# Optimization experiments

Hardware: AMD Instinct MI355X
Metric: run time of the kernel (lower is better)

## Reference

```python
import jax, jax.numpy as jnp
import numpy as np

EMBED_DIM = 1024
NUM_HEADS = 16
HEAD_DIM = EMBED_DIM // NUM_HEADS


def setup_inputs() -> dict:
    key = jax.random.key(0)
    ks = jax.random.split(key, 6)
    B, S = 2, 2048
    x = jax.random.normal(ks[0], (B, S, EMBED_DIM), dtype=jnp.float32)
    # causal boolean mask, broadcast to (B, H, S, S)
    causal = jnp.tril(jnp.ones((S, S), dtype=bool))
    mask = jnp.broadcast_to(causal, (B, NUM_HEADS, S, S))
    s_in = 1.0 / np.sqrt(EMBED_DIM)
    qkv_w = jax.random.normal(ks[1], (3 * EMBED_DIM, EMBED_DIM), dtype=jnp.float32) * s_in
    qkv_b = jax.random.normal(ks[2], (3 * EMBED_DIM,), dtype=jnp.float32) * 0.01
    proj_w = jax.random.normal(ks[3], (EMBED_DIM, EMBED_DIM), dtype=jnp.float32) * s_in
    proj_b = jax.random.normal(ks[4], (EMBED_DIM,), dtype=jnp.float32) * 0.01
    return {"x": x, "mask": mask, "qkv_w": qkv_w, "qkv_b": qkv_b,
            "proj_w": proj_w, "proj_b": proj_b}


def reference(x, mask, qkv_w, qkv_b, proj_w, proj_b):
    B, S, E = x.shape
    H, D = NUM_HEADS, HEAD_DIM
    qkv = x @ qkv_w.T + qkv_b                     # (B, S, 3E)
    q, k, v = jnp.split(qkv, 3, axis=-1)
    # (B, H, S, D)
    q = q.reshape(B, S, H, D).transpose(0, 2, 1, 3)
    k = k.reshape(B, S, H, D).transpose(0, 2, 1, 3)
    v = v.reshape(B, S, H, D).transpose(0, 2, 1, 3)
    scale = D ** (-0.5)
    attn = jnp.einsum('bhqd,bhkd->bhqk', q, k) * scale
    attn = jnp.where(mask, attn, jnp.float32(-10000.0))
    attn = attn - jnp.max(attn, axis=-1, keepdims=True)
    attn = jax.nn.softmax(attn, axis=-1)
    attn = jnp.where(mask, attn, jnp.float32(0.0))
    # dropout is identity in eval mode
    out = jnp.einsum('bhqk,bhkd->bhqd', attn, v)
    out = out.transpose(0, 2, 1, 3).reshape(B, S, E)
    return out @ proj_w.T + proj_b
```

## Files before the change

kernel.cpp:

```cpp
#include <hip/hip_runtime.h>
#include <hip/hip_bf16.h>

#define BATCH 2
#define SEQ 2048
#define EMBED 1024
#define NHEADS 16
#define HDIM 64

typedef __hip_bfloat16 bf16;
typedef __attribute__((ext_vector_type(8))) short bf16x8;
typedef __attribute__((ext_vector_type(4))) short bf16x4;
typedef __attribute__((ext_vector_type(4))) float f32x4;

typedef const __attribute__((address_space(1))) void* gaddr_t;
typedef __attribute__((address_space(3))) void* laddr_t;

__device__ __forceinline__ bf16x8 lds_frag8(const bf16* p) {
    const bf16x4 a = *(const bf16x4*)p;
    const bf16x4 b = *(const bf16x4*)(p + 4);
    return __builtin_shufflevector(a, b, 0, 1, 2, 3, 4, 5, 6, 7);
}

__global__ __launch_bounds__(256)
void f2b_all(const float* __restrict__ s0, bf16* __restrict__ d0, int n0,
             const float* __restrict__ s1, bf16* __restrict__ d1, int n1,
             const float* __restrict__ s2, bf16* __restrict__ d2, int n2)
{
    int i = blockIdx.x * 256 + threadIdx.x;
    const float* s; bf16* d;
    if (i < n0)                { s = s0; d = d0; }
    else if ((i -= n0) < n1)   { s = s1; d = d1; }
    else if ((i -= n1) < n2)   { s = s2; d = d2; }
    else return;
    const float4 v = ((const float4*)s)[i];
    union { ushort4 u4; bf16 h[4]; } o;
    o.h[0] = __float2bfloat16(v.x);
    o.h[1] = __float2bfloat16(v.y);
    o.h[2] = __float2bfloat16(v.z);
    o.h[3] = __float2bfloat16(v.w);
    ((ushort4*)d)[i] = o.u4;
}

template<int MODE>
__global__ __launch_bounds__(256)
void gemm_bt(const bf16* __restrict__ A, const bf16* __restrict__ B,
             const float* __restrict__ bias, void* __restrict__ Cv,
             int M, int N, int K)
{
    __shared__ __align__(16) bf16 lA[128 * 32];
    __shared__ __align__(16) bf16 lB[128 * 32];
    const int tid  = threadIdx.x;
    const int bn   = blockIdx.x, bm = blockIdx.y;
    const int wave = tid >> 6, lane = tid & 63;
    const int wm   = (wave >> 1) << 6, wn = (wave & 1) << 6;
    const int quad = lane >> 4, l16 = lane & 15;

    f32x4 acc[4][4] = {};

    for (int kt = 0; kt < K; kt += 32) {
        __syncthreads();
        #pragma unroll
        for (int i = 0; i < 2; ++i) {
            const int c = tid + (i << 8);
            const int r = c >> 2, kc = (c & 3) << 3;
            const bf16* gA = A + (long)(bm * 128 + r) * K + (kt + kc);
            const bf16* gB = B + (long)(bn * 128 + r) * K + (kt + kc);
            __builtin_amdgcn_global_load_lds((gaddr_t)gA, (laddr_t)&lA[c << 3], 16, 0, 0);
            __builtin_amdgcn_global_load_lds((gaddr_t)gB, (laddr_t)&lB[c << 3], 16, 0, 0);
        }
        __syncthreads();

        bf16x8 af[4], bfr[4];
        #pragma unroll
        for (int t = 0; t < 4; ++t) {
            af[t]  = *(const bf16x8*)&lA[(wm + t * 16 + l16) * 32 + quad * 8];
            bfr[t] = *(const bf16x8*)&lB[(wn + t * 16 + l16) * 32 + quad * 8];
        }
        #pragma unroll
        for (int tm = 0; tm < 4; ++tm)
            #pragma unroll
            for (int tn = 0; tn < 4; ++tn)
                acc[tm][tn] = __builtin_amdgcn_mfma_f32_16x16x32_bf16(
                    af[tm], bfr[tn], acc[tm][tn], 0, 0, 0);
    }

    #pragma unroll
    for (int tm = 0; tm < 4; ++tm) {
        #pragma unroll
        for (int tn = 0; tn < 4; ++tn) {
            const int gn = bn * 128 + wn + tn * 16 + l16;
            const float bv = bias[gn];
            if (MODE == 0) {
                #pragma unroll
                for (int r = 0; r < 4; ++r) {
                    const int gm = bm * 128 + wm + tm * 16 + quad * 4 + r;
                    ((float*)Cv)[(long)gm * N + gn] = acc[tm][tn][r] + bv;
                }
            } else {
                const int part = gn >> 10, h = (gn >> 6) & (NHEADS - 1), d = gn & (HDIM - 1);
                const int gm0 = bm * 128 + wm + tm * 16 + quad * 4;
                const int b = gm0 >> 11, s0 = gm0 & (SEQ - 1);
                if (part == 2) {
                    union { ushort4 u4; bf16 hv[4]; } o;
                    #pragma unroll
                    for (int r = 0; r < 4; ++r) o.hv[r] = __float2bfloat16(acc[tm][tn][r] + bv);
                    const long off = ((((long)2 * BATCH + b) * NHEADS + h) * HDIM + d) * SEQ + s0;
                    *(ushort4*)((bf16*)Cv + off) = o.u4;
                } else {
                    #pragma unroll
                    for (int r = 0; r < 4; ++r) {
                        const long off = ((((long)part * BATCH + b) * NHEADS + h) * SEQ + (s0 + r)) * HDIM + d;
                        ((bf16*)Cv)[off] = __float2bfloat16(acc[tm][tn][r] + bv);
                    }
                }
            }
        }
    }
}

__global__ __launch_bounds__(256)
void attn_nf(const bf16* __restrict__ Q, const bf16* __restrict__ K,
             const bf16* __restrict__ Vt, bf16* __restrict__ O)
{
    __shared__ __align__(16) bf16 pS[4 * 32 * 68];

    const int tid  = threadIdx.x;
    const int wave = tid >> 6, lane = tid & 63;
    const int quad = lane >> 4, l15 = lane & 15;
    const int bh   = blockIdx.y;
    const int qg   = (15 - blockIdx.x) * 4 + wave;
    const int qw0  = qg * 32;

    const bf16* Qb  = Q  + (long)bh * SEQ * HDIM;
    const bf16* Kb  = K  + (long)bh * SEQ * HDIM;
    const bf16* Vtb = Vt + (long)bh * HDIM * SEQ;
    bf16* pW = pS + wave * 32 * 68;

    bf16x8 qf[2][2];
    #pragma unroll
    for (int mt = 0; mt < 2; ++mt)
        #pragma unroll
        for (int c = 0; c < 2; ++c) {
            union { int4 i; bf16x8 v; } u;
            u.i = *(const int4*)(Qb + (long)(qw0 + mt * 16 + l15) * HDIM + c * 32 + quad * 8);
            qf[mt][c] = u.v;
        }

    f32x4 acc[2][4] = {};
    float lsum[8] = {};

    const int nkt = (qw0 >> 6) + 1;
    const float sc = 0.125f * 1.44269504088896340736f;

    for (int t = 0; t < nkt; ++t) {
        const int kb = t * 64;

        f32x4 s[2][4] = {};
        #pragma unroll
        for (int c = 0; c < 2; ++c) {
            #pragma unroll
            for (int nt = 0; nt < 4; ++nt) {
                union { int4 i; bf16x8 v; } u;
                u.i = *(const int4*)(Kb + (long)(kb + nt * 16 + l15) * HDIM + c * 32 + quad * 8);
                #pragma unroll
                for (int mt = 0; mt < 2; ++mt)
                    s[mt][nt] = __builtin_amdgcn_mfma_f32_16x16x32_bf16(
                        qf[mt][c], u.v, s[mt][nt], 0, 0, 0);
            }
        }

        #pragma unroll
        for (int mt = 0; mt < 2; ++mt)
            #pragma unroll
            for (int nt = 0; nt < 4; ++nt)
                #pragma unroll
                for (int r = 0; r < 4; ++r) {
                    const int rl = mt * 16 + quad * 4 + r;
                    const int cl = nt * 16 + l15;
                    const float p = ((kb + cl) <= (qw0 + rl))
                        ? __builtin_amdgcn_exp2f(s[mt][nt][r] * sc) : 0.f;
                    lsum[mt * 4 + r] += p;
                    pW[rl * 68 + cl] = __float2bfloat16(p);
                }

        #pragma unroll
        for (int c = 0; c < 2; ++c) {
            bf16x8 pf[2];
            #pragma unroll
            for (int mt = 0; mt < 2; ++mt)
                pf[mt] = lds_frag8(&pW[(mt * 16 + l15) * 68 + c * 32 + quad * 8]);
            #pragma unroll
            for (int nt = 0; nt < 4; ++nt) {
                union { int4 i; bf16x8 v; } u;
                u.i = *(const int4*)(Vtb + (long)(nt * 16 + l15) * SEQ + kb + c * 32 + quad * 8);
                #pragma unroll
                for (int mt = 0; mt < 2; ++mt)
                    acc[mt][nt] = __builtin_amdgcn_mfma_f32_16x16x32_bf16(
                        pf[mt], u.v, acc[mt][nt], 0, 0, 0);
            }
        }
    }

    #pragma unroll
    for (int i = 0; i < 8; ++i) {
        #pragma unroll
        for (int m = 1; m < 16; m <<= 1) lsum[i] += __shfl_xor(lsum[i], m, 64);
        lsum[i] = 1.f / lsum[i];
    }

    const int b = bh >> 4, h = bh & 15;
    #pragma unroll
    for (int mt = 0; mt < 2; ++mt)
        #pragma unroll
        for (int r = 0; r < 4; ++r) {
            const int rl = mt * 16 + quad * 4 + r;
            bf16* orow = O + ((long)b * SEQ + (qw0 + rl)) * EMBED + h * HDIM;
            const float inv = lsum[mt * 4 + r];
            #pragma unroll
            for (int nt = 0; nt < 4; ++nt)
                orow[nt * 16 + l15] = __float2bfloat16(acc[mt][nt][r] * inv);
        }
}

extern "C" void kernel_launch(void* const* d_in, const int* in_sizes, int n_in,
                              void* d_out, int out_size, void* d_ws, size_t ws_size,
                              hipStream_t stream)
{
    const float* x      = (const float*)d_in[0];
    const float* qkv_w  = (const float*)d_in[2];
    const float* qkv_b  = (const float*)d_in[3];
    const float* proj_w = (const float*)d_in[4];
    const float* proj_b = (const float*)d_in[5];
    float* out = (float*)d_out;

    const long nX  = (long)BATCH * SEQ * EMBED;
    const long nQW = 3L * EMBED * EMBED;
    const long nPW = (long)EMBED * EMBED;
    const long per = (long)BATCH * NHEADS * SEQ * HDIM;

    bf16* xw  = (bf16*)d_ws;
    bf16* qwm = xw + nX;
    bf16* pwm = qwm + nQW;
    bf16* qw  = pwm + nPW;
    bf16* kw  = qw + per;
    bf16* vw  = kw + per;
    bf16* att = vw + per;

    const int n0 = (int)(nX / 4), n1 = (int)(nQW / 4), n2 = (int)(nPW / 4);
    f2b_all<<<(n0 + n1 + n2 + 255) / 256, 256, 0, stream>>>(
        x, xw, n0, qkv_w, qwm, n1, proj_w, pwm, n2);

    gemm_bt<1><<<dim3(3 * EMBED / 128, BATCH * SEQ / 128), 256, 0, stream>>>(
        xw, qwm, qkv_b, qw, BATCH * SEQ, 3 * EMBED, EMBED);

    attn_nf<<<dim3(16, BATCH * NHEADS), 256, 0, stream>>>(qw, kw, vw, att);

    gemm_bt<0><<<dim3(EMBED / 128, BATCH * SEQ / 128), 256, 0, stream>>>(
        att, pwm, proj_b, out, BATCH * SEQ, EMBED, EMBED);
}
```

Baseline: 765.9 us.

## Split attention key loop across two blocks and combine partial outputs

Each attention query tile is now processed by two blocks, each taking alternate key tiles, which doubles the grid to improve CU occupancy and load balance. Unnormalized fp32 partial outputs and row sums go to workspace, and a new combine kernel adds them, normalizes, and writes bf16 in the head-interleaved layout. This trades extra global traffic and an additional launch for more parallelism.

```diff
diff --git a/kernel.cpp b/kernel.cpp
--- a/kernel.cpp
+++ b/kernel.cpp
@@ -120,15 +120,18 @@
 
 __global__ __launch_bounds__(256)
 void attn_nf(const bf16* __restrict__ Q, const bf16* __restrict__ K,
-             const bf16* __restrict__ Vt, bf16* __restrict__ O)
+             const bf16* __restrict__ Vt, float* __restrict__ Op,
+             float* __restrict__ lp)
 {
     __shared__ __align__(16) bf16 pS[4 * 32 * 68];
 
     const int tid  = threadIdx.x;
     const int wave = tid >> 6, lane = tid & 63;
     const int quad = lane >> 4, l15 = lane & 15;
-    const int bh   = blockIdx.y;
-    const int qg   = (15 - blockIdx.x) * 4 + wave;
+    const int bh   = blockIdx.x;
+    const int half = blockIdx.y >> 4;
+    const int qidx = blockIdx.y & 15;
+    const int qg   = (15 - qidx) * 4 + wave;
     const int qw0  = qg * 32;
 
     const bf16* Qb  = Q  + (long)bh * SEQ * HDIM;
@@ -152,7 +155,7 @@
     const int nkt = (qw0 >> 6) + 1;
     const float sc = 0.125f * 1.44269504088896340736f;
 
-    for (int t = 0; t < nkt; ++t) {
+    for (int t = half; t < nkt; t += 2) {
         const int kb = t * 64;
 
         f32x4 s[2][4] = {};
@@ -202,24 +205,45 @@
     }
 
     #pragma unroll
-    for (int i = 0; i < 8; ++i) {
+    for (int i = 0; i < 8; ++i)
         #pragma unroll
         for (int m = 1; m < 16; m <<= 1) lsum[i] += __shfl_xor(lsum[i], m, 64);
-        lsum[i] = 1.f / lsum[i];
-    }
-
-    const int b = bh >> 4, h = bh & 15;
+
+    const long halfO = (long)BATCH * NHEADS * SEQ * HDIM;
+    float* Oh = Op + half * halfO + ((long)bh * SEQ) * HDIM;
+    float* lh = lp + half * (BATCH * NHEADS * SEQ) + bh * SEQ;
     #pragma unroll
     for (int mt = 0; mt < 2; ++mt)
         #pragma unroll
         for (int r = 0; r < 4; ++r) {
             const int rl = mt * 16 + quad * 4 + r;
-            bf16* orow = O + ((long)b * SEQ + (qw0 + rl)) * EMBED + h * HDIM;
-            const float inv = lsum[mt * 4 + r];
+            float* orow = Oh + (long)(qw0 + rl) * HDIM;
             #pragma unroll
             for (int nt = 0; nt < 4; ++nt)
-                orow[nt * 16 + l15] = __float2bfloat16(acc[mt][nt][r] * inv);
-        }
+                orow[nt * 16 + l15] = acc[mt][nt][r];
+            if (l15 == 0) lh[qw0 + rl] = lsum[mt * 4 + r];
+        }
+}
+
+__global__ __launch_bounds__(256)
+void attn_combine(const float* __restrict__ Op, const float* __restrict__ lp,
+                  bf16* __restrict__ att)
+{
+    const int i = blockIdx.x * 256 + threadIdx.x;
+    const int d4 = i & 15, q = (i >> 4) & (SEQ - 1), bh = i >> 15;
+    const long halfO = (long)BATCH * NHEADS * SEQ * HDIM;
+    const long rowo  = ((long)bh * SEQ + q) * HDIM;
+    const float4 a = ((const float4*)(Op + rowo))[d4];
+    const float4 b = ((const float4*)(Op + halfO + rowo))[d4];
+    const int li = bh * SEQ + q;
+    const float inv = 1.f / (lp[li] + lp[BATCH * NHEADS * SEQ + li]);
+    const int bb = bh >> 4, h = bh & 15;
+    union { ushort4 u4; bf16 hv[4]; } o;
+    o.hv[0] = __float2bfloat16((a.x + b.x) * inv);
+    o.hv[1] = __float2bfloat16((a.y + b.y) * inv);
+    o.hv[2] = __float2bfloat16((a.z + b.z) * inv);
+    o.hv[3] = __float2bfloat16((a.w + b.w) * inv);
+    *(ushort4*)(att + ((long)bb * SEQ + q) * EMBED + h * HDIM + d4 * 4) = o.u4;
 }
 
 extern "C" void kernel_launch(void* const* d_in, const int* in_sizes, int n_in,
@@ -245,6 +269,8 @@
     bf16* kw  = qw + per;
     bf16* vw  = kw + per;
     bf16* att = vw + per;
+    float* Op = (float*)(att + per);
+    float* lp = Op + 2 * per;
 
     const int n0 = (int)(nX / 4), n1 = (int)(nQW / 4), n2 = (int)(nPW / 4);
     f2b_all<<<(n0 + n1 + n2 + 255) / 256, 256, 0, stream>>>(
@@ -253,7 +279,8 @@
     gemm_bt<1><<<dim3(3 * EMBED / 128, BATCH * SEQ / 128), 256, 0, stream>>>(
         xw, qwm, qkv_b, qw, BATCH * SEQ, 3 * EMBED, EMBED);
 
-    attn_nf<<<dim3(16, BATCH * NHEADS), 256, 0, stream>>>(qw, kw, vw, att);
+    attn_nf<<<dim3(BATCH * NHEADS, 32), 256, 0, stream>>>(qw, kw, vw, Op, lp);
+    attn_combine<<<(int)(per / 4 / 256), 256, 0, stream>>>(Op, lp, att);
 
     gemm_bt<0><<<dim3(EMBED / 128, BATCH * SEQ / 128), 256, 0, stream>>>(
         att, pwm, proj_b, out, BATCH * SEQ, EMBED, EMBED);
```

New measurement: 724.5 us (median of 2 runs). 5.4% less time.
